# Optimization experiments

Hardware: AMD Instinct MI355X
Metric: run time of the kernel (lower is better)

## Reference

```python
import jax, jax.numpy as jnp
import numpy as np

B, N, DIM, HEADS = 4, 2048, 512, 8
LN_EPS = 1e-5


def setup_inputs() -> dict:
    key = jax.random.key(0)
    ks = jax.random.split(key, 16)
    w = lambda k: jax.random.normal(k, (DIM, DIM), jnp.float32) * 0.02
    bv = lambda k: jax.random.normal(k, (DIM,), jnp.float32) * 0.02
    return {
        'x': jax.random.normal(ks[0], (B, N, DIM), jnp.float32),
        'y': jax.random.normal(ks[1], (B, N, DIM), jnp.float32),
        'Wq': w(ks[2]), 'bq': bv(ks[3]),
        'Wk': w(ks[4]), 'bk': bv(ks[5]),
        'Wvr': w(ks[6]), 'bvr': bv(ks[7]),
        'Wvd': w(ks[8]), 'bvd': bv(ks[9]),
        'g_r': jnp.ones((DIM,), jnp.float32), 'b_r': jnp.zeros((DIM,), jnp.float32),
        'g_d': jnp.ones((DIM,), jnp.float32), 'b_d': jnp.zeros((DIM,), jnp.float32),
        'Wpr': w(ks[10]), 'bpr': bv(ks[11]),
        'Wpd': w(ks[12]), 'bpd': bv(ks[13]),
        'num_heads': HEADS,
    }


def _ln(t, g, b):
    mu = jnp.mean(t, axis=-1, keepdims=True)
    var = jnp.mean(jnp.square(t - mu), axis=-1, keepdims=True)
    return (t - mu) * jax.lax.rsqrt(var + LN_EPS) * g + b


def reference(x, y, Wq, bq, Wk, bk, Wvr, bvr, Wvd, bvd,
              g_r, b_r, g_d, b_d, Wpr, bpr, Wpd, bpd, num_heads):
    Bn, Nn, C = x.shape
    D = C // num_heads
    xn = _ln(x, g_r, b_r)   # norm_r(x)
    yn = _ln(y, g_d, b_d)   # norm_d(y)

    def heads(t, W, b):  # Linear then split heads -> (B, H, N, D)
        return (t @ W.T + b).reshape(Bn, Nn, num_heads, D).transpose(0, 2, 1, 3)

    q_r = heads(yn, Wq, bq)    # query from depth-normed y
    v_r = heads(xn, Wvr, bvr)
    k_d = heads(xn, Wk, bk)
    v_d = heads(xn, Wvd, bvd)

    scale = D ** -0.5
    attn = jnp.einsum('bhnd,bhmd->bhnm', q_r, k_d) * scale  # shared QK^T
    attn_r = jax.nn.softmax(attn, axis=-1)                  # row-wise
    attn_d = jax.nn.softmax(attn.transpose(0, 1, 3, 2), axis=-1)  # col-wise (transposed)

    out_r = jnp.einsum('bhnm,bhmd->bhnd', attn_r, v_r)
    out_r = out_r.transpose(0, 2, 1, 3).reshape(Bn, Nn, C) @ Wpr.T + bpr

    o_d = jnp.einsum('bhnm,bhmd->bhnd', attn_d, v_d)
    o_d = o_d.transpose(0, 2, 1, 3).reshape(Bn, Nn, C)
    # Faithful to source quirk: extra transpose(1,2)+reshape scrambles layout.
    o_d = o_d.transpose(0, 2, 1).reshape(Bn, Nn, C)
    out_d = o_d @ Wpd.T + bpd
    return out_r, out_d
```

## Files before the change

kernel.cpp:

```cpp
#include <hip/hip_runtime.h>
#include <hip/hip_bf16.h>

typedef __hip_bfloat16 bf16;
typedef __attribute__((ext_vector_type(8))) short short8;
typedef __attribute__((ext_vector_type(4))) short short4v;
typedef __attribute__((ext_vector_type(4))) float floatx4;

static constexpr int B = 4;
static constexpr int N = 2048;
static constexpr int C = 512;
static constexpr int H = 8;
static constexpr int D = 64;

#define QK_SCALE 0.18033688011112042f

__device__ int g_flags[18];

__device__ __forceinline__ float u2f(unsigned short u) {
    return __uint_as_float(((unsigned int)u) << 16);
}
__device__ __forceinline__ unsigned short f2bf(float f) {
    unsigned int u = __float_as_uint(f);
    return (unsigned short)((u + 0x7FFFu + ((u >> 16) & 1u)) >> 16);
}
__device__ __forceinline__ float ldin(const void* p, size_t i, int f) {
    if (f == 2) return 0.0f;
    return f ? ((const float*)p)[i] : u2f(((const unsigned short*)p)[i]);
}

__device__ __forceinline__ void ld8(const void* p, size_t idx, int f, float* o) {
    if (f == 1) {
        const float4* q = (const float4*)((const float*)p + idx);
        float4 a = q[0], b2 = q[1];
        o[0] = a.x; o[1] = a.y; o[2] = a.z; o[3] = a.w;
        o[4] = b2.x; o[5] = b2.y; o[6] = b2.z; o[7] = b2.w;
    } else if (f == 0) {
        short8 s8 = *(const short8*)((const unsigned short*)p + idx);
        #pragma unroll
        for (int i = 0; i < 8; ++i) o[i] = u2f((unsigned short)s8[i]);
    } else {
        #pragma unroll
        for (int i = 0; i < 8; ++i) o[i] = 0.0f;
    }
}

__device__ __forceinline__ void gl_lds16(const unsigned short* g, unsigned short* l) {
    __builtin_amdgcn_global_load_lds(
        (const __attribute__((address_space(1))) unsigned int*)g,
        (__attribute__((address_space(3))) unsigned int*)l,
        16, 0, 0);
}

struct Ptrs { const void* p[18]; };

__global__ void detect_kernel(Ptrs ptrs) {
    int t = blockIdx.x;
    int lane = threadIdx.x;
    unsigned int v = ((const unsigned int*)ptrs.p[t])[lane];
    unsigned int e = (v >> 7) & 0xFF;
    unsigned long long mp = __ballot(e >= 96 && e <= 144);
    unsigned long long mz = __ballot(v != 0u);
    if (lane == 0)
        g_flags[t] = (mz == 0ull) ? 2 : ((__popcll(mp) >= 32) ? 0 : 1);
}

__global__ __launch_bounds__(256) void convert_w(Ptrs ptrs, bf16* dst) {
    int wsel = blockIdx.y;
    int wi = wsel < 4 ? 2 + 2 * wsel : 14 + 2 * (wsel - 4);
    int f = g_flags[wi];
    const void* src = ptrs.p[wi];
    unsigned short* out = (unsigned short*)dst + (size_t)wsel * 262144;
    int base = (blockIdx.x * 256 + threadIdx.x) * 16;
    if (f == 1) {
        const float4* s = (const float4*)((const float*)src + base);
        float4 f0 = s[0], f1 = s[1], f2 = s[2], f3 = s[3];
        uint4 o0, o1;
        o0.x = f2bf(f0.x) | ((unsigned int)f2bf(f0.y) << 16);
        o0.y = f2bf(f0.z) | ((unsigned int)f2bf(f0.w) << 16);
        o0.z = f2bf(f1.x) | ((unsigned int)f2bf(f1.y) << 16);
        o0.w = f2bf(f1.z) | ((unsigned int)f2bf(f1.w) << 16);
        o1.x = f2bf(f2.x) | ((unsigned int)f2bf(f2.y) << 16);
        o1.y = f2bf(f2.z) | ((unsigned int)f2bf(f2.w) << 16);
        o1.z = f2bf(f3.x) | ((unsigned int)f2bf(f3.y) << 16);
        o1.w = f2bf(f3.z) | ((unsigned int)f2bf(f3.w) << 16);
        *(uint4*)(out + base) = o0;
        *(uint4*)(out + base + 8) = o1;
    } else if (f == 0) {
        const uint4* s = (const uint4*)((const unsigned short*)src + base);
        uint4 a = s[0], b2 = s[1];
        *(uint4*)(out + base) = a;
        *(uint4*)(out + base + 8) = b2;
    } else {
        uint4 z = {0, 0, 0, 0};
        *(uint4*)(out + base) = z;
        *(uint4*)(out + base + 8) = z;
    }
}

__global__ __launch_bounds__(256) void ln_kernel(
    const void* __restrict__ x, const void* __restrict__ y,
    const void* __restrict__ g_r, const void* __restrict__ b_r,
    const void* __restrict__ g_d, const void* __restrict__ b_d,
    bf16* __restrict__ xn, bf16* __restrict__ yn)
{
    int tid = threadIdx.x;
    int wid = tid >> 6, lane = tid & 63;
    int row = blockIdx.x * 4 + wid;
    bool isY = row >= B * N;
    int r = isY ? row - B * N : row;
    const void* src = isY ? y : x;
    int sf = isY ? g_flags[1] : g_flags[0];
    const void* g  = isY ? g_d : g_r;
    int gf = isY ? g_flags[12] : g_flags[10];
    const void* bb = isY ? b_d : b_r;
    int bflag = isY ? g_flags[13] : g_flags[11];
    bf16* dst = (isY ? yn : xn) + (size_t)r * C;

    int col = lane * 8;
    float v[8];
    ld8(src, (size_t)r * C + col, sf, v);

    float s = 0.f, sq = 0.f;
    #pragma unroll
    for (int i = 0; i < 8; ++i) { s += v[i]; sq += v[i] * v[i]; }
    #pragma unroll
    for (int off = 1; off < 64; off <<= 1) {
        s  += __shfl_xor(s, off);
        sq += __shfl_xor(sq, off);
    }
    float mu = s * (1.0f / C);
    float var = sq * (1.0f / C) - mu * mu;
    float rs = rsqrtf(var + 1e-5f);

    float gv[8], bv[8];
    ld8(g, col, gf, gv);
    ld8(bb, col, bflag, bv);

    union { unsigned short us[8]; short8 s8; } o;
    #pragma unroll
    for (int i = 0; i < 8; ++i)
        o.us[i] = f2bf((v[i] - mu) * rs * gv[i] + bv[i]);
    *(short8*)(dst + col) = o.s8;
}

__device__ __forceinline__ void gemm_core(
    const bf16* __restrict__ A, const bf16* __restrict__ W,
    const void* __restrict__ bias, int bflag, void* __restrict__ Cout,
    int omode, float oscale, int n0, int m0)
{
    __shared__ __align__(16) unsigned short As[2][128 * 64];
    __shared__ __align__(16) unsigned short Ws[2][64 * 64];

    int tid = threadIdx.x;
    int wave = tid >> 6, lane = tid & 63;
    int wm = (wave >> 1) * 64, wn = (wave & 1) * 32;
    int quad = lane >> 4, mr = lane & 15;
    int m8 = mr & 7;

    floatx4 acc[4][2] = {};

    const unsigned short* Asrc[4];
    const unsigned short* Wsrc[2];
    #pragma unroll
    for (int i = 0; i < 4; ++i) {
        int c = i * 256 + tid, row = c >> 3, sg = c & 7;
        Asrc[i] = (const unsigned short*)A + (size_t)(m0 + row) * 512 + ((sg ^ (row & 7)) << 3);
    }
    #pragma unroll
    for (int j = 0; j < 2; ++j) {
        int c = j * 256 + tid, row = c >> 3, sg = c & 7;
        Wsrc[j] = (const unsigned short*)W + (size_t)(n0 + row) * 512 + ((sg ^ (row & 7)) << 3);
    }

    auto STAGE = [&](int w, int bsel) {
        int ko = w * 64;
        #pragma unroll
        for (int i = 0; i < 4; ++i)
            gl_lds16(Asrc[i] + ko, &As[bsel][(i * 256 + tid) * 8]);
        #pragma unroll
        for (int j = 0; j < 2; ++j)
            gl_lds16(Wsrc[j] + ko, &Ws[bsel][(j * 256 + tid) * 8]);
    };

    auto WBODY = [&](int bsel, int w) {
        asm volatile("s_waitcnt vmcnt(0)" ::: "memory");
        __builtin_amdgcn_s_barrier();
        if (w < 7)
            STAGE(w + 1, bsel ^ 1);
        __builtin_amdgcn_sched_barrier(0);

        #pragma unroll
        for (int kk = 0; kk < 2; ++kk) {
            int sl = ((kk * 4 + quad) ^ m8) << 3;
            short8 af[4], bfr[2];
            #pragma unroll
            for (int i = 0; i < 4; ++i)
                af[i] = *(const short8*)&As[bsel][(wm + i * 16 + mr) * 64 + sl];
            #pragma unroll
            for (int j = 0; j < 2; ++j)
                bfr[j] = *(const short8*)&Ws[bsel][(wn + j * 16 + mr) * 64 + sl];
            #pragma unroll
            for (int i = 0; i < 4; ++i)
                #pragma unroll
                for (int j = 0; j < 2; ++j)
                    acc[i][j] = __builtin_amdgcn_mfma_f32_16x16x32_bf16(
                        af[i], bfr[j], acc[i][j], 0, 0, 0);
        }
        __builtin_amdgcn_sched_barrier(0);
    };

    STAGE(0, 0);
    #pragma unroll
    for (int g = 0; g < 4; ++g) {
        WBODY(0, 2 * g);
        WBODY(1, 2 * g + 1);
    }

    float bv[2];
    #pragma unroll
    for (int j = 0; j < 2; ++j)
        bv[j] = ldin(bias, n0 + wn + j * 16 + mr, bflag);
    #pragma unroll
    for (int i = 0; i < 4; ++i) {
        #pragma unroll
        for (int j = 0; j < 2; ++j) {
            int o = n0 + wn + j * 16 + mr;
            #pragma unroll
            for (int reg = 0; reg < 4; ++reg) {
                int r = m0 + wm + i * 16 + quad * 4 + reg;
                float val = (acc[i][j][reg] + bv[j]) * oscale;
                if (omode == 0) {
                    ((bf16*)Cout)[(size_t)r * 512 + o] = __float2bfloat16(val);
                } else if (omode == 1) {
                    ((float*)Cout)[(size_t)r * 512 + o] = val;
                } else {
                    int batch = r >> 11, nn = r & 2047;
                    ((bf16*)Cout)[((size_t)(batch * 512 + o)) * 2048 + nn] =
                        __float2bfloat16(val);
                }
            }
        }
    }
}

__device__ __forceinline__ void swz_nm(int& n0, int& m0) {
    m0 = (blockIdx.x * 8 + (blockIdx.y >> 3)) * 128;
    n0 = (blockIdx.y & 7) * 64;
}

__global__ __launch_bounds__(256, 3) void gemm_stage(
    const bf16* __restrict__ xn, const bf16* __restrict__ yn,
    const bf16* __restrict__ wts, Ptrs ptrs,
    bf16* __restrict__ q, bf16* __restrict__ k,
    bf16* __restrict__ vrT, bf16* __restrict__ vdT)
{
    int z = blockIdx.z;
    const bf16* A = (z == 0) ? yn : xn;
    const bf16* W = wts + (size_t)z * 262144;
    int bi = 3 + 2 * z;
    void* Cout = (z == 0) ? (void*)q : (z == 1) ? (void*)k
               : (z == 2) ? (void*)vrT : (void*)vdT;
    int omode = (z < 2) ? 0 : 2;
    float oscale = (z == 0) ? QK_SCALE : 1.0f;
    int n0, m0;
    swz_nm(n0, m0);
    gemm_core(A, W, ptrs.p[bi], g_flags[bi], Cout, omode, oscale, n0, m0);
}

__global__ __launch_bounds__(256, 3) void gemm_out(
    const bf16* __restrict__ Or, const bf16* __restrict__ Ad,
    const bf16* __restrict__ wts, Ptrs ptrs,
    float* __restrict__ out0, float* __restrict__ out1)
{
    int z = blockIdx.z;
    const bf16* A = z ? Ad : Or;
    const bf16* W = wts + (size_t)(4 + z) * 262144;
    int bi = 15 + 2 * z;
    int n0, m0;
    swz_nm(n0, m0);
    gemm_core(A, W, ptrs.p[bi], g_flags[bi], z ? (void*)out1 : (void*)out0,
              1, 1.0f, n0, m0);
}

__global__ __launch_bounds__(512, 8) void flash_mfma(
    const bf16* __restrict__ qm, const bf16* __restrict__ km,
    const bf16* __restrict__ vrT, const bf16* __restrict__ vdT,
    bf16* __restrict__ Or, bf16* __restrict__ Ad)
{
    __shared__ __align__(16) unsigned short Ks[2][64 * 64];
    __shared__ __align__(16) unsigned short Vs[2][64 * 64];

    int phys = blockIdx.x + 16 * blockIdx.y + 128 * blockIdx.z;
    int s = phys >> 3;
    int qblk = s & 15;
    int gidx = (phys & 7) + ((s >> 4) << 3);
    int pass = gidx >> 5;
    int b = (gidx >> 3) & 3;
    int h = gidx & 7;

    const bf16* Q  = pass ? km : qm;
    const bf16* K  = pass ? qm : km;
    const bf16* Vt = pass ? vdT : vrT;
    bf16* Out = pass ? Ad : Or;

    int tid = threadIdx.x;
    int wave = tid >> 6, lane = tid & 63;
    int quad = lane >> 4, mr = lane & 15;
    int m8 = mr & 7;
    int qw = qblk * 128 + wave * 16;

    const unsigned short* Qb = (const unsigned short*)Q + ((size_t)(b * N + qw + mr)) * C + h * D;
    short8 qf0 = *(const short8*)(Qb + quad * 8);
    short8 qf1 = *(const short8*)(Qb + 32 + quad * 8);

    floatx4 Oacc[4] = {};
    floatx4 lacc = {};

    short4v ones;
    {
        union { unsigned int u[2]; short4v s4; } cv;
        cv.u[0] = 0x3F803F80u; cv.u[1] = 0x3F803F80u;
        ones = cv.s4;
    }

    int r0 = tid >> 3, cs0 = tid & 7;
    const unsigned short* Kb  = (const unsigned short*)K + ((size_t)b * N) * C + h * D;
    const unsigned short* Vtb = (const unsigned short*)Vt + ((size_t)(b * 512 + h * 64)) * 2048;
    const unsigned short* sk0 = Kb + (size_t)r0 * C + ((cs0 ^ (r0 & 7)) << 3);
    const unsigned short* sv0 = Vtb + (size_t)r0 * 2048 + ((cs0 ^ (r0 & 7)) << 3);

    auto STAGE = [&](int bsel) {
        gl_lds16(sk0, &Ks[bsel][tid * 8]);
        gl_lds16(sv0, &Vs[bsel][tid * 8]);
        sk0 += 64 * C; sv0 += 64;
    };

    int skc0 = (quad ^ m8) << 3;
    int skc1 = ((quad + 4) ^ m8) << 3;
    int vq = quad >> 1, vlo = (quad & 1) * 4;

    auto BODY = [&](int cur, bool last) {
        asm volatile("s_waitcnt vmcnt(0)" ::: "memory");
        __builtin_amdgcn_s_barrier();
        if (!last)
            STAGE(cur ^ 1);
        __builtin_amdgcn_sched_barrier(0);

        floatx4 tac[4] = {};
        __builtin_amdgcn_s_setprio(1);
        #pragma unroll
        for (int t = 0; t < 4; ++t) {
            const unsigned short* kr = &Ks[cur][(t * 16 + mr) * 64];
            short8 kf0 = *(const short8*)(kr + skc0);
            short8 kf1 = *(const short8*)(kr + skc1);
            tac[t] = __builtin_amdgcn_mfma_f32_16x16x32_bf16(kf0, qf0, tac[t], 0, 0, 0);
            tac[t] = __builtin_amdgcn_mfma_f32_16x16x32_bf16(kf1, qf1, tac[t], 0, 0, 0);
        }
        __builtin_amdgcn_s_setprio(0);

        short4v pa[4];
        #pragma unroll
        for (int t = 0; t < 4; ++t) {
            float p0, p1, p2, p3;
            asm("v_exp_f32 %0, %1" : "=v"(p0) : "v"(tac[t][0]));
            asm("v_exp_f32 %0, %1" : "=v"(p1) : "v"(tac[t][1]));
            asm("v_exp_f32 %0, %1" : "=v"(p2) : "v"(tac[t][2]));
            asm("v_exp_f32 %0, %1" : "=v"(p3) : "v"(tac[t][3]));
            unsigned int u0, u1;
            asm("v_cvt_pk_bf16_f32 %0, %1, %2" : "=v"(u0) : "v"(p0), "v"(p1));
            asm("v_cvt_pk_bf16_f32 %0, %1, %2" : "=v"(u1) : "v"(p2), "v"(p3));
            union { unsigned int u[2]; short4v s4; } cv;
            cv.u[0] = u0; cv.u[1] = u1;
            pa[t] = cv.s4;
        }

        __builtin_amdgcn_s_setprio(1);
        #pragma unroll
        for (int t = 0; t < 4; ++t) {
            int vslot = (((2 * t + vq) ^ m8) << 3) + vlo;
            #pragma unroll
            for (int j = 0; j < 4; ++j) {
                short4v vb = *(const short4v*)&Vs[cur][(j * 16 + mr) * 64 + vslot];
                Oacc[j] = __builtin_amdgcn_mfma_f32_16x16x16bf16_1k(
                    pa[t], vb, Oacc[j], 0, 0, 0);
            }
            lacc = __builtin_amdgcn_mfma_f32_16x16x16bf16_1k(pa[t], ones, lacc, 0, 0, 0);
        }
        __builtin_amdgcn_s_setprio(0);
        __builtin_amdgcn_sched_barrier(0);
    };

    STAGE(0);
    for (int kt2 = 0; kt2 < 15; ++kt2) {
        BODY(0, false);
        BODY(1, false);
    }
    BODY(0, false);
    BODY(1, true);

    float inv[4];
    #pragma unroll
    for (int r = 0; r < 4; ++r)
        inv[r] = 1.0f / lacc[r];

    if (pass == 0) {
        #pragma unroll
        for (int t = 0; t < 4; ++t)
            #pragma unroll
            for (int r = 0; r < 4; ++r) {
                int n = qw + quad * 4 + r;
                Out[((size_t)(b * N + n)) * C + h * D + t * 16 + mr] =
                    __float2bfloat16(Oacc[t][r] * inv[r]);
            }
    } else {
        size_t bbase = (size_t)b * N * C;
        #pragma unroll
        for (int t = 0; t < 4; ++t)
            #pragma unroll
            for (int r = 0; r < 4; ++r) {
                int n = qw + quad * 4 + r;
                int c = h * D + t * 16 + mr;
                Out[bbase + (size_t)(c * 4 + (n >> 9)) * 512 + (n & 511)] =
                    __float2bfloat16(Oacc[t][r] * inv[r]);
            }
    }
}

extern "C" void kernel_launch(void* const* d_in, const int* in_sizes, int n_in,
                              void* d_out, int out_size, void* d_ws, size_t ws_size,
                              hipStream_t stream)
{
    const void* x   = d_in[0];
    const void* y   = d_in[1];
    const void* g_r = d_in[10];
    const void* b_r = d_in[11];
    const void* g_d = d_in[12];
    const void* b_d = d_in[13];

    Ptrs ptrs;
    for (int i = 0; i < 18; ++i) ptrs.p[i] = d_in[i];

    const size_t SL = (size_t)B * N * C;

    char* wsb = (char*)d_ws;
    bf16* q   = (bf16*)wsb;
    bf16* k   = (bf16*)(wsb + 8ull * 1024 * 1024);
    bf16* vrT = (bf16*)(wsb + 16ull * 1024 * 1024);
    bf16* vdT = (bf16*)(wsb + 24ull * 1024 * 1024);
    bf16* xn  = (bf16*)(wsb + 32ull * 1024 * 1024);
    bf16* yn  = (bf16*)(wsb + 40ull * 1024 * 1024);
    bf16* wts = (bf16*)(wsb + 48ull * 1024 * 1024);
    bf16* Or = xn;
    bf16* Ad = yn;

    float* out0 = (float*)d_out;
    float* out1 = (float*)d_out + SL;

    detect_kernel<<<18, 64, 0, stream>>>(ptrs);
    convert_w<<<dim3(64, 6), 256, 0, stream>>>(ptrs, wts);
    ln_kernel<<<2 * B * N / 4, 256, 0, stream>>>(x, y, g_r, b_r, g_d, b_d, xn, yn);

    gemm_stage<<<dim3(8, 64, 4), 256, 0, stream>>>(xn, yn, wts, ptrs, q, k, vrT, vdT);

    dim3 fg(16, 8, 8);
    flash_mfma<<<fg, 512, 0, stream>>>(q, k, vrT, vdT, Or, Ad);

    gemm_out<<<dim3(8, 64, 2), 256, 0, stream>>>(Or, Ad, wts, ptrs, out0, out1);
}
```

Baseline: 264.8 us.

## Enlarge GEMM tiles to 128x128 and process two query blocks per flash wave

The GEMM kernels move from 128x64 to 128x128 output tiles: each wave now computes 64x64, with a new XCD-aware block mapping and a launch-bounds occupancy hint of 2. The flash attention kernel has each wave handle two 16-row query groups that share one set of K/V LDS fragments, which halves the grid and the K/V staging per query row. The aim is more MFMA work per LDS read and per global load. The cost is higher register pressure, lower occupancy and fewer blocks to fill the CUs.

```diff
diff --git a/kernel.cpp b/kernel.cpp
--- a/kernel.cpp
+++ b/kernel.cpp
@@ -149,37 +149,32 @@
     int omode, float oscale, int n0, int m0)
 {
     __shared__ __align__(16) unsigned short As[2][128 * 64];
-    __shared__ __align__(16) unsigned short Ws[2][64 * 64];
+    __shared__ __align__(16) unsigned short Ws[2][128 * 64];
 
     int tid = threadIdx.x;
     int wave = tid >> 6, lane = tid & 63;
-    int wm = (wave >> 1) * 64, wn = (wave & 1) * 32;
+    int wm = (wave >> 1) * 64, wn = (wave & 1) * 64;
     int quad = lane >> 4, mr = lane & 15;
     int m8 = mr & 7;
 
-    floatx4 acc[4][2] = {};
+    floatx4 acc[4][4] = {};
 
     const unsigned short* Asrc[4];
-    const unsigned short* Wsrc[2];
+    const unsigned short* Wsrc[4];
     #pragma unroll
     for (int i = 0; i < 4; ++i) {
         int c = i * 256 + tid, row = c >> 3, sg = c & 7;
         Asrc[i] = (const unsigned short*)A + (size_t)(m0 + row) * 512 + ((sg ^ (row & 7)) << 3);
-    }
-    #pragma unroll
-    for (int j = 0; j < 2; ++j) {
-        int c = j * 256 + tid, row = c >> 3, sg = c & 7;
-        Wsrc[j] = (const unsigned short*)W + (size_t)(n0 + row) * 512 + ((sg ^ (row & 7)) << 3);
+        Wsrc[i] = (const unsigned short*)W + (size_t)(n0 + row) * 512 + ((sg ^ (row & 7)) << 3);
     }
 
     auto STAGE = [&](int w, int bsel) {
         int ko = w * 64;
         #pragma unroll
-        for (int i = 0; i < 4; ++i)
+        for (int i = 0; i < 4; ++i) {
             gl_lds16(Asrc[i] + ko, &As[bsel][(i * 256 + tid) * 8]);
-        #pragma unroll
-        for (int j = 0; j < 2; ++j)
-            gl_lds16(Wsrc[j] + ko, &Ws[bsel][(j * 256 + tid) * 8]);
+            gl_lds16(Wsrc[i] + ko, &Ws[bsel][(i * 256 + tid) * 8]);
+        }
     };
 
     auto WBODY = [&](int bsel, int w) {
@@ -192,17 +187,17 @@
         #pragma unroll
         for (int kk = 0; kk < 2; ++kk) {
             int sl = ((kk * 4 + quad) ^ m8) << 3;
-            short8 af[4], bfr[2];
+            short8 af[4], bfr[4];
             #pragma unroll
             for (int i = 0; i < 4; ++i)
                 af[i] = *(const short8*)&As[bsel][(wm + i * 16 + mr) * 64 + sl];
             #pragma unroll
-            for (int j = 0; j < 2; ++j)
+            for (int j = 0; j < 4; ++j)
                 bfr[j] = *(const short8*)&Ws[bsel][(wn + j * 16 + mr) * 64 + sl];
             #pragma unroll
             for (int i = 0; i < 4; ++i)
                 #pragma unroll
-                for (int j = 0; j < 2; ++j)
+                for (int j = 0; j < 4; ++j)
                     acc[i][j] = __builtin_amdgcn_mfma_f32_16x16x32_bf16(
                         af[i], bfr[j], acc[i][j], 0, 0, 0);
         }
@@ -216,14 +211,14 @@
         WBODY(1, 2 * g + 1);
     }
 
-    float bv[2];
-    #pragma unroll
-    for (int j = 0; j < 2; ++j)
+    float bv[4];
+    #pragma unroll
+    for (int j = 0; j < 4; ++j)
         bv[j] = ldin(bias, n0 + wn + j * 16 + mr, bflag);
     #pragma unroll
     for (int i = 0; i < 4; ++i) {
         #pragma unroll
-        for (int j = 0; j < 2; ++j) {
+        for (int j = 0; j < 4; ++j) {
             int o = n0 + wn + j * 16 + mr;
             #pragma unroll
             for (int reg = 0; reg < 4; ++reg) {
@@ -244,11 +239,14 @@
 }
 
 __device__ __forceinline__ void swz_nm(int& n0, int& m0) {
-    m0 = (blockIdx.x * 8 + (blockIdx.y >> 3)) * 128;
-    n0 = (blockIdx.y & 7) * 64;
-}
-
-__global__ __launch_bounds__(256, 3) void gemm_stage(
+    int lid = blockIdx.x + 4 * blockIdx.y;
+    int xcd = lid & 7;
+    int grp = lid >> 3;
+    m0 = (xcd * 8 + (grp >> 2)) * 128;
+    n0 = (grp & 3) * 128;
+}
+
+__global__ __launch_bounds__(256, 2) void gemm_stage(
     const bf16* __restrict__ xn, const bf16* __restrict__ yn,
     const bf16* __restrict__ wts, Ptrs ptrs,
     bf16* __restrict__ q, bf16* __restrict__ k,
@@ -267,7 +265,7 @@
     gemm_core(A, W, ptrs.p[bi], g_flags[bi], Cout, omode, oscale, n0, m0);
 }
 
-__global__ __launch_bounds__(256, 3) void gemm_out(
+__global__ __launch_bounds__(256, 2) void gemm_out(
     const bf16* __restrict__ Or, const bf16* __restrict__ Ad,
     const bf16* __restrict__ wts, Ptrs ptrs,
     float* __restrict__ out0, float* __restrict__ out1)
@@ -282,7 +280,7 @@
               1, 1.0f, n0, m0);
 }
 
-__global__ __launch_bounds__(512, 8) void flash_mfma(
+__global__ __launch_bounds__(512, 4) void flash_mfma(
     const bf16* __restrict__ qm, const bf16* __restrict__ km,
     const bf16* __restrict__ vrT, const bf16* __restrict__ vdT,
     bf16* __restrict__ Or, bf16* __restrict__ Ad)
@@ -290,10 +288,10 @@
     __shared__ __align__(16) unsigned short Ks[2][64 * 64];
     __shared__ __align__(16) unsigned short Vs[2][64 * 64];
 
-    int phys = blockIdx.x + 16 * blockIdx.y + 128 * blockIdx.z;
+    int phys = blockIdx.x + 8 * blockIdx.y + 64 * blockIdx.z;
     int s = phys >> 3;
-    int qblk = s & 15;
-    int gidx = (phys & 7) + ((s >> 4) << 3);
+    int qblk = s & 7;
+    int gidx = (phys & 7) | ((s >> 3) << 3);
     int pass = gidx >> 5;
     int b = (gidx >> 3) & 3;
     int h = gidx & 7;
@@ -307,14 +305,18 @@
     int wave = tid >> 6, lane = tid & 63;
     int quad = lane >> 4, mr = lane & 15;
     int m8 = mr & 7;
-    int qw = qblk * 128 + wave * 16;
-
-    const unsigned short* Qb = (const unsigned short*)Q + ((size_t)(b * N + qw + mr)) * C + h * D;
-    short8 qf0 = *(const short8*)(Qb + quad * 8);
-    short8 qf1 = *(const short8*)(Qb + 32 + quad * 8);
-
-    floatx4 Oacc[4] = {};
-    floatx4 lacc = {};
+    int qw = qblk * 256 + wave * 16;
+
+    const unsigned short* Qb0 = (const unsigned short*)Q + ((size_t)(b * N + qw + mr)) * C + h * D;
+    const unsigned short* Qb1 = Qb0 + (size_t)128 * C;
+    short8 qa0 = *(const short8*)(Qb0 + quad * 8);
+    short8 qa1 = *(const short8*)(Qb0 + 32 + quad * 8);
+    short8 qb0 = *(const short8*)(Qb1 + quad * 8);
+    short8 qb1 = *(const short8*)(Qb1 + 32 + quad * 8);
+
+    floatx4 OaccA[4] = {};
+    floatx4 OaccB[4] = {};
+    floatx4 la = {}, lb = {};
 
     short4v ones;
     {
@@ -346,32 +348,38 @@
             STAGE(cur ^ 1);
         __builtin_amdgcn_sched_barrier(0);
 
-        floatx4 tac[4] = {};
-        __builtin_amdgcn_s_setprio(1);
+        short4v pa[4], pb[4];
         #pragma unroll
         for (int t = 0; t < 4; ++t) {
             const unsigned short* kr = &Ks[cur][(t * 16 + mr) * 64];
             short8 kf0 = *(const short8*)(kr + skc0);
             short8 kf1 = *(const short8*)(kr + skc1);
-            tac[t] = __builtin_amdgcn_mfma_f32_16x16x32_bf16(kf0, qf0, tac[t], 0, 0, 0);
-            tac[t] = __builtin_amdgcn_mfma_f32_16x16x32_bf16(kf1, qf1, tac[t], 0, 0, 0);
-        }
-        __builtin_amdgcn_s_setprio(0);
-
-        short4v pa[4];
-        #pragma unroll
-        for (int t = 0; t < 4; ++t) {
-            float p0, p1, p2, p3;
-            asm("v_exp_f32 %0, %1" : "=v"(p0) : "v"(tac[t][0]));
-            asm("v_exp_f32 %0, %1" : "=v"(p1) : "v"(tac[t][1]));
-            asm("v_exp_f32 %0, %1" : "=v"(p2) : "v"(tac[t][2]));
-            asm("v_exp_f32 %0, %1" : "=v"(p3) : "v"(tac[t][3]));
-            unsigned int u0, u1;
-            asm("v_cvt_pk_bf16_f32 %0, %1, %2" : "=v"(u0) : "v"(p0), "v"(p1));
-            asm("v_cvt_pk_bf16_f32 %0, %1, %2" : "=v"(u1) : "v"(p2), "v"(p3));
-            union { unsigned int u[2]; short4v s4; } cv;
-            cv.u[0] = u0; cv.u[1] = u1;
-            pa[t] = cv.s4;
+            __builtin_amdgcn_s_setprio(1);
+            floatx4 ta = {}, tb = {};
+            ta = __builtin_amdgcn_mfma_f32_16x16x32_bf16(kf0, qa0, ta, 0, 0, 0);
+            ta = __builtin_amdgcn_mfma_f32_16x16x32_bf16(kf1, qa1, ta, 0, 0, 0);
+            tb = __builtin_amdgcn_mfma_f32_16x16x32_bf16(kf0, qb0, tb, 0, 0, 0);
+            tb = __builtin_amdgcn_mfma_f32_16x16x32_bf16(kf1, qb1, tb, 0, 0, 0);
+            __builtin_amdgcn_s_setprio(0);
+            float e0, e1, e2, e3, f0, f1, f2, f3;
+            asm("v_exp_f32 %0, %1" : "=v"(e0) : "v"(ta[0]));
+            asm("v_exp_f32 %0, %1" : "=v"(e1) : "v"(ta[1]));
+            asm("v_exp_f32 %0, %1" : "=v"(e2) : "v"(ta[2]));
+            asm("v_exp_f32 %0, %1" : "=v"(e3) : "v"(ta[3]));
+            asm("v_exp_f32 %0, %1" : "=v"(f0) : "v"(tb[0]));
+            asm("v_exp_f32 %0, %1" : "=v"(f1) : "v"(tb[1]));
+            asm("v_exp_f32 %0, %1" : "=v"(f2) : "v"(tb[2]));
+            asm("v_exp_f32 %0, %1" : "=v"(f3) : "v"(tb[3]));
+            unsigned int ua0, ua1, ub0, ub1;
+            asm("v_cvt_pk_bf16_f32 %0, %1, %2" : "=v"(ua0) : "v"(e0), "v"(e1));
+            asm("v_cvt_pk_bf16_f32 %0, %1, %2" : "=v"(ua1) : "v"(e2), "v"(e3));
+            asm("v_cvt_pk_bf16_f32 %0, %1, %2" : "=v"(ub0) : "v"(f0), "v"(f1));
+            asm("v_cvt_pk_bf16_f32 %0, %1, %2" : "=v"(ub1) : "v"(f2), "v"(f3));
+            union { unsigned int u[2]; short4v s4; } ca, cb;
+            ca.u[0] = ua0; ca.u[1] = ua1;
+            cb.u[0] = ub0; cb.u[1] = ub1;
+            pa[t] = ca.s4;
+            pb[t] = cb.s4;
         }
 
         __builtin_amdgcn_s_setprio(1);
@@ -381,10 +389,13 @@
             #pragma unroll
             for (int j = 0; j < 4; ++j) {
                 short4v vb = *(const short4v*)&Vs[cur][(j * 16 + mr) * 64 + vslot];
-                Oacc[j] = __builtin_amdgcn_mfma_f32_16x16x16bf16_1k(
-                    pa[t], vb, Oacc[j], 0, 0, 0);
+                OaccA[j] = __builtin_amdgcn_mfma_f32_16x16x16bf16_1k(
+                    pa[t], vb, OaccA[j], 0, 0, 0);
+                OaccB[j] = __builtin_amdgcn_mfma_f32_16x16x16bf16_1k(
+                    pb[t], vb, OaccB[j], 0, 0, 0);
             }
-            lacc = __builtin_amdgcn_mfma_f32_16x16x16bf16_1k(pa[t], ones, lacc, 0, 0, 0);
+            la = __builtin_amdgcn_mfma_f32_16x16x16bf16_1k(pa[t], ones, la, 0, 0, 0);
+            lb = __builtin_amdgcn_mfma_f32_16x16x16bf16_1k(pb[t], ones, lb, 0, 0, 0);
         }
         __builtin_amdgcn_s_setprio(0);
         __builtin_amdgcn_sched_barrier(0);
@@ -398,10 +409,12 @@
     BODY(0, false);
     BODY(1, true);
 
-    float inv[4];
-    #pragma unroll
-    for (int r = 0; r < 4; ++r)
-        inv[r] = 1.0f / lacc[r];
+    float inva[4], invb[4];
+    #pragma unroll
+    for (int r = 0; r < 4; ++r) {
+        inva[r] = 1.0f / la[r];
+        invb[r] = 1.0f / lb[r];
+    }
 
     if (pass == 0) {
         #pragma unroll
@@ -410,7 +423,9 @@
             for (int r = 0; r < 4; ++r) {
                 int n = qw + quad * 4 + r;
                 Out[((size_t)(b * N + n)) * C + h * D + t * 16 + mr] =
-                    __float2bfloat16(Oacc[t][r] * inv[r]);
+                    __float2bfloat16(OaccA[t][r] * inva[r]);
+                Out[((size_t)(b * N + n + 128)) * C + h * D + t * 16 + mr] =
+                    __float2bfloat16(OaccB[t][r] * invb[r]);
             }
     } else {
         size_t bbase = (size_t)b * N * C;
@@ -421,7 +436,10 @@
                 int n = qw + quad * 4 + r;
                 int c = h * D + t * 16 + mr;
                 Out[bbase + (size_t)(c * 4 + (n >> 9)) * 512 + (n & 511)] =
-                    __float2bfloat16(Oacc[t][r] * inv[r]);
+                    __float2bfloat16(OaccA[t][r] * inva[r]);
+                int n2 = n + 128;
+                Out[bbase + (size_t)(c * 4 + (n2 >> 9)) * 512 + (n2 & 511)] =
+                    __float2bfloat16(OaccB[t][r] * invb[r]);
             }
     }
 }
@@ -460,10 +478,10 @@
     convert_w<<<dim3(64, 6), 256, 0, stream>>>(ptrs, wts);
     ln_kernel<<<2 * B * N / 4, 256, 0, stream>>>(x, y, g_r, b_r, g_d, b_d, xn, yn);
 
-    gemm_stage<<<dim3(8, 64, 4), 256, 0, stream>>>(xn, yn, wts, ptrs, q, k, vrT, vdT);
-
-    dim3 fg(16, 8, 8);
+    gemm_stage<<<dim3(4, 64, 4), 256, 0, stream>>>(xn, yn, wts, ptrs, q, k, vrT, vdT);
+
+    dim3 fg(8, 8, 8);
     flash_mfma<<<fg, 512, 0, stream>>>(q, k, vrT, vdT, Or, Ad);
 
-    gemm_out<<<dim3(8, 64, 2), 256, 0, stream>>>(Or, Ad, wts, ptrs, out0, out1);
-}
+    gemm_out<<<dim3(4, 64, 2), 256, 0, stream>>>(Or, Ad, wts, ptrs, out0, out1);
+}
```

New measurement: 257.5 us. 1.03x faster.
